# Optimization experiments

Measured on AMD Instinct MI355X. Metric: run time of the kernel, lower is better.

Reference implementation:

```python
import jax, jax.numpy as jnp
import numpy as np

B, S, D, H = 2, 2048, 1024, 16
MASK_VAL = -50000.0

def setup_inputs() -> dict:
    key = jax.random.key(0)
    k1, k2, k3, k4 = jax.random.split(key, 4)
    # weights stored as [in, out] so projection is x @ W (equals torch Linear with W.T)
    s = 1.0 / np.sqrt(D)
    return {
        "x": jax.random.normal(k1, (B, S, D), dtype=jnp.float32),
        "Wq": jax.random.normal(k2, (D, D), dtype=jnp.float32) * s,
        "Wkv": jax.random.normal(k3, (D, 2 * D), dtype=jnp.float32) * s,
        "Wo": jax.random.normal(k4, (D, D), dtype=jnp.float32) * s,
    }

def reference(x, Wq, Wkv, Wo):
    b, sl, d = x.shape
    h = H
    hd = d // h
    scale = hd ** (-0.5)
    q = x @ Wq                      # [b, sl, d]
    kv = x @ Wkv                    # [b, sl, 2d]
    k, v = jnp.split(kv, 2, axis=-1)
    # [b, h, s, hd]
    q = q.reshape(b, sl, h, hd).transpose(0, 2, 1, 3)
    k = k.reshape(b, sl, h, hd).transpose(0, 2, 1, 3)
    v = v.reshape(b, sl, h, hd).transpose(0, 2, 1, 3)
    dots = jnp.einsum('bhid,bhjd->bhij', q * scale, k)  # [b,h,s,s]
    # causal: strictly-upper-triangular entries set to MASK_VAL
    causal = jnp.tril(jnp.ones((sl, sl), dtype=bool))
    dots = jnp.where(causal, dots, MASK_VAL)
    attn = jax.nn.softmax(dots, axis=-1)
    out = jnp.einsum('bhij,bhjd->bihd', attn, v).reshape(b, sl, d)
    return out @ Wo
```

## Files before the change

kernel.cpp:

```cpp
#include <hip/hip_runtime.h>

typedef __bf16 bf16_t;
typedef unsigned short u16;
typedef __attribute__((ext_vector_type(8))) __bf16 bf16x8;
typedef __attribute__((ext_vector_type(4))) float f32x4;
typedef __attribute__((ext_vector_type(4))) u16 u16x4;
typedef __attribute__((ext_vector_type(8))) u16 u16x8;

#define SS 2048
#define PSTR 72

__device__ __forceinline__ u16 f2b(float f) {
    return __builtin_bit_cast(u16, (__bf16)f);
}

__device__ __forceinline__ void async_copy16(const u16* g, u16* l) {
    __builtin_amdgcn_global_load_lds(
        (__attribute__((address_space(1))) void*)(u16*)g,
        (__attribute__((address_space(3))) void*)l, 16, 0, 0);
}

__device__ __forceinline__ bf16x8 ldfrag(const u16* p) {
    return __builtin_bit_cast(bf16x8, *(const u16x8*)p);
}

__global__ __launch_bounds__(256)
void cast_x_kernel(const float* __restrict__ x, u16* __restrict__ xb) {
    size_t i = ((size_t)blockIdx.x * 256 + threadIdx.x) * 8;
    float4 a = *(const float4*)(x + i);
    float4 b = *(const float4*)(x + i + 4);
    u16x8 o;
    o[0] = f2b(a.x); o[1] = f2b(a.y); o[2] = f2b(a.z); o[3] = f2b(a.w);
    o[4] = f2b(b.x); o[5] = f2b(b.y); o[6] = f2b(b.z); o[7] = f2b(b.w);
    *(u16x8*)(xb + i) = o;
}

__global__ __launch_bounds__(256)
void transpose_all(const float* __restrict__ Wq, const float* __restrict__ Wkv,
                   const float* __restrict__ Wo, u16* __restrict__ WcatT,
                   u16* __restrict__ WoT) {
    const int z = blockIdx.z;
    if (z != 1 && blockIdx.y >= 16) return;
    const float* src; u16* dst; int N; float scale;
    if (z == 0)      { src = Wq;  dst = WcatT;               N = 1024; scale = 0.125f * 1.44269504089f; }
    else if (z == 1) { src = Wkv; dst = WcatT + 1024 * 1024; N = 2048; scale = 1.0f; }
    else             { src = Wo;  dst = WoT;                 N = 1024; scale = 1.0f; }
    __shared__ __attribute__((aligned(16))) u16 tile[64][72];
    const int k0 = blockIdx.x * 64, n0 = blockIdx.y * 64;
    const int tid = threadIdx.x;
#pragma unroll
    for (int p = 0; p < 4; ++p) {
        int c = p * 256 + tid;
        int r = c >> 4, c4 = c & 15;
        float4 v = *(const float4*)(src + (size_t)(k0 + r) * N + n0 + c4 * 4);
        u16x4 o;
        o[0] = f2b(v.x * scale); o[1] = f2b(v.y * scale);
        o[2] = f2b(v.z * scale); o[3] = f2b(v.w * scale);
        *(u16x4*)&tile[r][c4 * 4] = o;
    }
    __syncthreads();
#pragma unroll
    for (int p = 0; p < 4; ++p) {
        int c = p * 256 + tid;
        int n = c >> 4, k4 = c & 15;
        u16x4 o;
#pragma unroll
        for (int i = 0; i < 4; ++i) o[i] = tile[k4 * 4 + i][n];
        *(u16x4*)(dst + (size_t)(n0 + n) * 1024 + k0 + k4 * 4) = o;
    }
}

__global__ __launch_bounds__(256)
void transpose_v(const u16* __restrict__ QKV, u16* __restrict__ VTg) {
    __shared__ __attribute__((aligned(16))) u16 tile[64][72];
    const int s0 = blockIdx.x * 64;
    const int bh = blockIdx.y;
    const int b = bh >> 4, h = bh & 15;
    const int tid = threadIdx.x;
    const u16* src = QKV + ((size_t)b * SS + s0) * 3072 + 2048 + h * 64;
#pragma unroll
    for (int p = 0; p < 4; ++p) {
        int c = p * 256 + tid;
        int s = c >> 4, h4 = c & 15;
        *(u16x4*)&tile[s][h4 * 4] = *(const u16x4*)(src + (size_t)s * 3072 + h4 * 4);
    }
    __syncthreads();
    u16* dst = VTg + (size_t)bh * 64 * 2048 + s0;
#pragma unroll
    for (int p = 0; p < 4; ++p) {
        int c = p * 256 + tid;
        int hd = c >> 4, s4 = c & 15;
        u16x4 o;
#pragma unroll
        for (int i = 0; i < 4; ++i) o[i] = tile[s4 * 4 + i][hd];
        *(u16x4*)(dst + (size_t)hd * 2048 + s4 * 4) = o;
    }
}

template <typename OutT>
__global__ __launch_bounds__(256, 2)
void gemm_bt(const u16* __restrict__ A, const u16* __restrict__ BT,
             OutT* __restrict__ C, int M, int N, int K) {
    __shared__ __attribute__((aligned(16))) u16 As[128 * 32];
    __shared__ __attribute__((aligned(16))) u16 Bs[128 * 32];
    const int tid = threadIdx.x;
    const int wave = tid >> 6, lane = tid & 63;
    const int l15 = lane & 15, quad = lane >> 4;
    const int m0 = blockIdx.y * 128, n0 = blockIdx.x * 128;
    const int wm = (wave >> 1) * 64, wn = (wave & 1) * 64;
    const f32x4 zero = {0.f, 0.f, 0.f, 0.f};
    f32x4 acc[4][4];
#pragma unroll
    for (int i = 0; i < 4; ++i)
#pragma unroll
        for (int j = 0; j < 4; ++j) acc[i][j] = zero;
    const int r0 = tid >> 2, kc = (tid & 3) * 8;
    for (int k0 = 0; k0 < K; k0 += 32) {
        async_copy16(A + (size_t)(m0 + r0) * K + k0 + kc, As + tid * 8);
        async_copy16(BT + (size_t)(n0 + r0) * K + k0 + kc, Bs + tid * 8);
        async_copy16(A + (size_t)(m0 + 64 + r0) * K + k0 + kc, As + (256 + tid) * 8);
        async_copy16(BT + (size_t)(n0 + 64 + r0) * K + k0 + kc, Bs + (256 + tid) * 8);
        __syncthreads();
        bf16x8 af[4], bf[4];
#pragma unroll
        for (int t = 0; t < 4; ++t) {
            af[t] = ldfrag(As + (wm + t * 16 + l15) * 32 + quad * 8);
            bf[t] = ldfrag(Bs + (wn + t * 16 + l15) * 32 + quad * 8);
        }
#pragma unroll
        for (int mt = 0; mt < 4; ++mt)
#pragma unroll
            for (int nt = 0; nt < 4; ++nt)
                acc[mt][nt] = __builtin_amdgcn_mfma_f32_16x16x32_bf16(
                    af[mt], bf[nt], acc[mt][nt], 0, 0, 0);
        __syncthreads();
    }
#pragma unroll
    for (int mt = 0; mt < 4; ++mt)
#pragma unroll
        for (int nt = 0; nt < 4; ++nt) {
            const int n = n0 + wn + nt * 16 + l15;
#pragma unroll
            for (int r = 0; r < 4; ++r) {
                const int m = m0 + wm + mt * 16 + quad * 4 + r;
                float v = acc[mt][nt][r];
                if constexpr (sizeof(OutT) == 2) C[(size_t)m * N + n] = (OutT)f2b(v);
                else                             C[(size_t)m * N + n] = v;
            }
        }
}

__device__ __forceinline__ void attn_score_softmax(
    const bf16x8 (&qf)[2], const bf16x8 (&kf)[4][2],
    float (&l_i)[4], u16* __restrict__ P, int wq, int kv0, int l15, int quad) {
    const f32x4 cinit = {-10.f, -10.f, -10.f, -10.f};
    f32x4 S[4];
#pragma unroll
    for (int nt = 0; nt < 4; ++nt) {
        f32x4 a = __builtin_amdgcn_mfma_f32_16x16x32_bf16(qf[0], kf[nt][0], cinit, 0, 0, 0);
        S[nt] = __builtin_amdgcn_mfma_f32_16x16x32_bf16(qf[1], kf[nt][1], a, 0, 0, 0);
    }
    if (kv0 + 63 > wq) {
#pragma unroll
        for (int nt = 0; nt < 4; ++nt)
#pragma unroll
            for (int r = 0; r < 4; ++r) {
                int qa = wq + quad * 4 + r;
                int ka = kv0 + nt * 16 + l15;
                if (ka > qa) S[nt][r] = -1e30f;
            }
    }
#pragma unroll
    for (int nt = 0; nt < 4; ++nt)
#pragma unroll
        for (int r = 0; r < 4; ++r) {
            float pv = exp2f(S[nt][r]);
            l_i[r] += pv;
            P[(quad * 4 + r) * PSTR + nt * 16 + l15] = f2b(pv);
        }
}

__device__ __forceinline__ void attn_pv(
    const u16* __restrict__ P, const bf16x8 (&vf)[4][2],
    f32x4 (&O)[4], int l15, int quad) {
    bf16x8 pf0 = ldfrag(P + l15 * PSTR + quad * 8);
    bf16x8 pf1 = ldfrag(P + l15 * PSTR + 32 + quad * 8);
#pragma unroll
    for (int nt = 0; nt < 4; ++nt) {
        O[nt] = __builtin_amdgcn_mfma_f32_16x16x32_bf16(pf0, vf[nt][0], O[nt], 0, 0, 0);
        O[nt] = __builtin_amdgcn_mfma_f32_16x16x32_bf16(pf1, vf[nt][1], O[nt], 0, 0, 0);
    }
}

__global__ __launch_bounds__(256, 2)
void attn_kernel(const u16* __restrict__ QKV, const u16* __restrict__ VTg,
                 u16* __restrict__ AO) {
    __shared__ __attribute__((aligned(16))) u16 Kt[2][2 * 64 * 32];
    __shared__ __attribute__((aligned(16))) u16 Vt[2][2 * 64 * 32];
    __shared__ __attribute__((aligned(16))) u16 Pq[128 * PSTR];
    const int tid = threadIdx.x;
    const int wave = tid >> 6, lane = tid & 63;
    const int l15 = lane & 15, quad = lane >> 4;
    const int bh = blockIdx.y, b = bh >> 4, h = bh & 15;
    const int xe = b ? 15 - (int)blockIdx.x : (int)blockIdx.x;
    const int qbA = 31 - xe, qbB = xe;
    const int qA0 = qbA * 64, qB0 = qbB * 64;
    const size_t bS = (size_t)b * SS;
    const u16* vbase = VTg + (size_t)bh * 64 * 2048;
    const int rr = (tid >> 2) & 63, kc8 = (tid & 3) * 8;

    {
        const u16* qsrcA = QKV + (bS + qA0 + rr) * 3072 + h * 64 + kc8;
        async_copy16(qsrcA,      Pq + tid * 8);
        async_copy16(qsrcA + 32, Pq + (256 + tid) * 8);
        const u16* qsrcB = QKV + (bS + qB0 + rr) * 3072 + h * 64 + kc8;
        async_copy16(qsrcB,      Pq + (512 + tid) * 8);
        async_copy16(qsrcB + 32, Pq + (768 + tid) * 8);
        const u16* ksrc = QKV + (bS + rr) * 3072 + 1024 + h * 64 + kc8;
        async_copy16(ksrc,      Kt[0] + tid * 8);
        async_copy16(ksrc + 32, Kt[0] + (256 + tid) * 8);
        const u16* vsrc = vbase + (size_t)rr * 2048 + kc8;
        async_copy16(vsrc,      Vt[0] + tid * 8);
        async_copy16(vsrc + 32, Vt[0] + (256 + tid) * 8);
    }
    __syncthreads();
    bf16x8 qfA[2], qfB[2];
#pragma unroll
    for (int ks = 0; ks < 2; ++ks) {
        qfA[ks] = ldfrag(Pq + ks * 2048 + (wave * 16 + l15) * 32 + quad * 8);
        qfB[ks] = ldfrag(Pq + 4096 + ks * 2048 + (wave * 16 + l15) * 32 + quad * 8);
    }
    __syncthreads();

    const int wqA = qA0 + wave * 16, wqB = qB0 + wave * 16;
    u16* PA = Pq + (wave * 16) * PSTR;
    u16* PB = Pq + (64 + wave * 16) * PSTR;
    float lA[4], lB[4];
    f32x4 OA[4], OB[4];
    const f32x4 zero = {0.f, 0.f, 0.f, 0.f};
#pragma unroll
    for (int r = 0; r < 4; ++r) { lA[r] = lB[r] = 0.f; }
#pragma unroll
    for (int nt = 0; nt < 4; ++nt) { OA[nt] = zero; OB[nt] = zero; }

    for (int j = 0; j <= qbA; ++j) {
        if (j < qbA) {
            const int kv1 = (j + 1) * 64;
            const int nb = (j + 1) & 1;
            const u16* ksrc = QKV + (bS + kv1 + rr) * 3072 + 1024 + h * 64 + kc8;
            async_copy16(ksrc,      Kt[nb] + tid * 8);
            async_copy16(ksrc + 32, Kt[nb] + (256 + tid) * 8);
            const u16* vsrc = vbase + (size_t)rr * 2048 + kv1 + kc8;
            async_copy16(vsrc,      Vt[nb] + tid * 8);
            async_copy16(vsrc + 32, Vt[nb] + (256 + tid) * 8);
        }
        const int kv0 = j * 64;
        const bool bAct = (j <= qbB);
        const u16* KB = Kt[j & 1];
        const u16* VB = Vt[j & 1];
        bf16x8 kf[4][2];
#pragma unroll
        for (int nt = 0; nt < 4; ++nt)
#pragma unroll
            for (int ks = 0; ks < 2; ++ks)
                kf[nt][ks] = ldfrag(KB + ks * 2048 + (nt * 16 + l15) * 32 + quad * 8);
        attn_score_softmax(qfA, kf, lA, PA, wqA, kv0, l15, quad);
        if (bAct)
            attn_score_softmax(qfB, kf, lB, PB, wqB, kv0, l15, quad);
        bf16x8 vf[4][2];
#pragma unroll
        for (int nt = 0; nt < 4; ++nt)
#pragma unroll
            for (int ks = 0; ks < 2; ++ks)
                vf[nt][ks] = ldfrag(VB + ks * 2048 + (nt * 16 + l15) * 32 + quad * 8);
        attn_pv(PA, vf, OA, l15, quad);
        if (bAct)
            attn_pv(PB, vf, OB, l15, quad);
        __syncthreads();
    }
#pragma unroll
    for (int r = 0; r < 4; ++r) {
        float sA = lA[r];
        sA += __shfl_xor(sA, 1); sA += __shfl_xor(sA, 2);
        sA += __shfl_xor(sA, 4); sA += __shfl_xor(sA, 8);
        float sB = lB[r];
        sB += __shfl_xor(sB, 1); sB += __shfl_xor(sB, 2);
        sB += __shfl_xor(sB, 4); sB += __shfl_xor(sB, 8);
        float invA = 1.0f / sA;
        float invB = 1.0f / sB;
        size_t rowA = bS + (size_t)wqA + quad * 4 + r;
        size_t rowB = bS + (size_t)wqB + quad * 4 + r;
#pragma unroll
        for (int nt = 0; nt < 4; ++nt) {
            AO[rowA * 1024 + h * 64 + nt * 16 + l15] = f2b(OA[nt][r] * invA);
            AO[rowB * 1024 + h * 64 + nt * 16 + l15] = f2b(OB[nt][r] * invB);
        }
    }
}

extern "C" void kernel_launch(void* const* d_in, const int* in_sizes, int n_in,
                              void* d_out, int out_size, void* d_ws, size_t ws_size,
                              hipStream_t stream) {
    (void)in_sizes; (void)n_in; (void)out_size; (void)ws_size;
    const float* x   = (const float*)d_in[0];
    const float* Wq  = (const float*)d_in[1];
    const float* Wkv = (const float*)d_in[2];
    const float* Wo  = (const float*)d_in[3];
    float* out = (float*)d_out;
    char* ws = (char*)d_ws;
    u16* xb    = (u16*)(ws);
    u16* WcatT = (u16*)(ws + (size_t)(8 << 20));
    u16* WoT   = (u16*)(ws + (size_t)(14 << 20));
    u16* QKV   = (u16*)(ws + (size_t)(16 << 20));
    u16* VTb   = (u16*)(ws + (size_t)(40 << 20));
    u16* AO    = xb;

    cast_x_kernel<<<2048, 256, 0, stream>>>(x, xb);
    transpose_all<<<dim3(16, 32, 3), 256, 0, stream>>>(Wq, Wkv, Wo, WcatT, WoT);
    gemm_bt<u16><<<dim3(24, 32), 256, 0, stream>>>(xb, WcatT, QKV, 4096, 3072, 1024);
    transpose_v<<<dim3(32, 32), 256, 0, stream>>>(QKV, VTb);
    attn_kernel<<<dim3(16, 32), 256, 0, stream>>>(QKV, VTb, AO);
    gemm_bt<float><<<dim3(8, 32), 256, 0, stream>>>(AO, WoT, out, 4096, 1024, 1024);
}
```

Baseline: 195.4 us.

## Split attention KV range across two blocks and add combine kernel

Each attention block pair is split into two halves over the key/value range, doubling the grid and raising the occupancy hint to 4 blocks per CU. Each half writes unnormalized bf16 partial outputs and row sums, and a new combine kernel adds them and normalizes. K/V staging drops from double-buffered prefetch to a single buffer that is loaded and synchronized each iteration, trading latency hiding for lower LDS use. The extra kernel and partial-output traffic add memory cost, and rounding the partials to bf16 adds rounding error.

Measured after the change: 205.5 us. +5.2%, slower.

```diff
diff --git a/kernel.cpp b/kernel.cpp
--- a/kernel.cpp
+++ b/kernel.cpp
@@ -12,6 +12,11 @@
 
 __device__ __forceinline__ u16 f2b(float f) {
     return __builtin_bit_cast(u16, (__bf16)f);
+}
+
+__device__ __forceinline__ float b2f(u16 v) {
+    unsigned u = (unsigned)v << 16;
+    return __builtin_bit_cast(float, u);
 }
 
 __device__ __forceinline__ void async_copy16(const u16* g, u16* l) {
@@ -192,19 +197,23 @@
     }
 }
 
-__global__ __launch_bounds__(256, 2)
+__global__ __launch_bounds__(256, 4)
 void attn_kernel(const u16* __restrict__ QKV, const u16* __restrict__ VTg,
-                 u16* __restrict__ AO) {
-    __shared__ __attribute__((aligned(16))) u16 Kt[2][2 * 64 * 32];
-    __shared__ __attribute__((aligned(16))) u16 Vt[2][2 * 64 * 32];
+                 u16* __restrict__ Opart, float* __restrict__ lpart) {
+    __shared__ __attribute__((aligned(16))) u16 Kt[2 * 64 * 32];
+    __shared__ __attribute__((aligned(16))) u16 Vt[2 * 64 * 32];
     __shared__ __attribute__((aligned(16))) u16 Pq[128 * PSTR];
     const int tid = threadIdx.x;
     const int wave = tid >> 6, lane = tid & 63;
     const int l15 = lane & 15, quad = lane >> 4;
     const int bh = blockIdx.y, b = bh >> 4, h = bh & 15;
-    const int xe = b ? 15 - (int)blockIdx.x : (int)blockIdx.x;
+    const int pair = (int)blockIdx.x >> 1, half = (int)blockIdx.x & 1;
+    const int xe = b ? 15 - pair : pair;
     const int qbA = 31 - xe, qbB = xe;
     const int qA0 = qbA * 64, qB0 = qbB * 64;
+    const int m = (xe >= 8) ? 8 : (15 - xe);
+    const int j0 = half ? m : 0;
+    const int j1 = half ? (qbA + 1) : m;
     const size_t bS = (size_t)b * SS;
     const u16* vbase = VTg + (size_t)bh * 64 * 2048;
     const int rr = (tid >> 2) & 63, kc8 = (tid & 3) * 8;
@@ -216,12 +225,6 @@
         const u16* qsrcB = QKV + (bS + qB0 + rr) * 3072 + h * 64 + kc8;
         async_copy16(qsrcB,      Pq + (512 + tid) * 8);
         async_copy16(qsrcB + 32, Pq + (768 + tid) * 8);
-        const u16* ksrc = QKV + (bS + rr) * 3072 + 1024 + h * 64 + kc8;
-        async_copy16(ksrc,      Kt[0] + tid * 8);
-        async_copy16(ksrc + 32, Kt[0] + (256 + tid) * 8);
-        const u16* vsrc = vbase + (size_t)rr * 2048 + kc8;
-        async_copy16(vsrc,      Vt[0] + tid * 8);
-        async_copy16(vsrc + 32, Vt[0] + (256 + tid) * 8);
     }
     __syncthreads();
     bf16x8 qfA[2], qfB[2];
@@ -243,27 +246,24 @@
 #pragma unroll
     for (int nt = 0; nt < 4; ++nt) { OA[nt] = zero; OB[nt] = zero; }
 
-    for (int j = 0; j <= qbA; ++j) {
-        if (j < qbA) {
-            const int kv1 = (j + 1) * 64;
-            const int nb = (j + 1) & 1;
-            const u16* ksrc = QKV + (bS + kv1 + rr) * 3072 + 1024 + h * 64 + kc8;
-            async_copy16(ksrc,      Kt[nb] + tid * 8);
-            async_copy16(ksrc + 32, Kt[nb] + (256 + tid) * 8);
-            const u16* vsrc = vbase + (size_t)rr * 2048 + kv1 + kc8;
-            async_copy16(vsrc,      Vt[nb] + tid * 8);
-            async_copy16(vsrc + 32, Vt[nb] + (256 + tid) * 8);
-        }
+    for (int j = j0; j < j1; ++j) {
         const int kv0 = j * 64;
+        {
+            const u16* ksrc = QKV + (bS + kv0 + rr) * 3072 + 1024 + h * 64 + kc8;
+            async_copy16(ksrc,      Kt + tid * 8);
+            async_copy16(ksrc + 32, Kt + (256 + tid) * 8);
+            const u16* vsrc = vbase + (size_t)rr * 2048 + kv0 + kc8;
+            async_copy16(vsrc,      Vt + tid * 8);
+            async_copy16(vsrc + 32, Vt + (256 + tid) * 8);
+        }
+        __syncthreads();
         const bool bAct = (j <= qbB);
-        const u16* KB = Kt[j & 1];
-        const u16* VB = Vt[j & 1];
         bf16x8 kf[4][2];
 #pragma unroll
         for (int nt = 0; nt < 4; ++nt)
 #pragma unroll
             for (int ks = 0; ks < 2; ++ks)
-                kf[nt][ks] = ldfrag(KB + ks * 2048 + (nt * 16 + l15) * 32 + quad * 8);
+                kf[nt][ks] = ldfrag(Kt + ks * 2048 + (nt * 16 + l15) * 32 + quad * 8);
         attn_score_softmax(qfA, kf, lA, PA, wqA, kv0, l15, quad);
         if (bAct)
             attn_score_softmax(qfB, kf, lB, PB, wqB, kv0, l15, quad);
@@ -272,12 +272,14 @@
         for (int nt = 0; nt < 4; ++nt)
 #pragma unroll
             for (int ks = 0; ks < 2; ++ks)
-                vf[nt][ks] = ldfrag(VB + ks * 2048 + (nt * 16 + l15) * 32 + quad * 8);
+                vf[nt][ks] = ldfrag(Vt + ks * 2048 + (nt * 16 + l15) * 32 + quad * 8);
         attn_pv(PA, vf, OA, l15, quad);
         if (bAct)
             attn_pv(PB, vf, OB, l15, quad);
         __syncthreads();
     }
+    u16* OpH = Opart + (size_t)half * 4096 * 1024;
+    float* lpH = lpart + (size_t)half * 4096 * 16;
 #pragma unroll
     for (int r = 0; r < 4; ++r) {
         float sA = lA[r];
@@ -286,16 +288,34 @@
         float sB = lB[r];
         sB += __shfl_xor(sB, 1); sB += __shfl_xor(sB, 2);
         sB += __shfl_xor(sB, 4); sB += __shfl_xor(sB, 8);
-        float invA = 1.0f / sA;
-        float invB = 1.0f / sB;
         size_t rowA = bS + (size_t)wqA + quad * 4 + r;
         size_t rowB = bS + (size_t)wqB + quad * 4 + r;
+        if (l15 == 0) {
+            lpH[rowA * 16 + h] = sA;
+            lpH[rowB * 16 + h] = sB;
+        }
 #pragma unroll
         for (int nt = 0; nt < 4; ++nt) {
-            AO[rowA * 1024 + h * 64 + nt * 16 + l15] = f2b(OA[nt][r] * invA);
-            AO[rowB * 1024 + h * 64 + nt * 16 + l15] = f2b(OB[nt][r] * invB);
-        }
-    }
+            OpH[rowA * 1024 + h * 64 + nt * 16 + l15] = f2b(OA[nt][r]);
+            OpH[rowB * 1024 + h * 64 + nt * 16 + l15] = f2b(OB[nt][r]);
+        }
+    }
+}
+
+__global__ __launch_bounds__(256)
+void combine_kernel(const u16* __restrict__ Opart, const float* __restrict__ lpart,
+                    u16* __restrict__ AO) {
+    const size_t idx = ((size_t)blockIdx.x * 256 + threadIdx.x) * 8;
+    const int row = (int)(idx >> 10);
+    const int head = (int)((idx & 1023) >> 6);
+    float l = lpart[row * 16 + head] + lpart[(size_t)4096 * 16 + row * 16 + head];
+    float inv = 1.0f / l;
+    u16x8 a = *(const u16x8*)(Opart + idx);
+    u16x8 c = *(const u16x8*)(Opart + (size_t)4096 * 1024 + idx);
+    u16x8 o;
+#pragma unroll
+    for (int i = 0; i < 8; ++i) o[i] = f2b((b2f(a[i]) + b2f(c[i])) * inv);
+    *(u16x8*)(AO + idx) = o;
 }
 
 extern "C" void kernel_launch(void* const* d_in, const int* in_sizes, int n_in,
@@ -313,12 +333,15 @@
     u16* WoT   = (u16*)(ws + (size_t)(14 << 20));
     u16* QKV   = (u16*)(ws + (size_t)(16 << 20));
     u16* VTb   = (u16*)(ws + (size_t)(40 << 20));
+    u16* Opart = (u16*)(ws + (size_t)(48 << 20));
+    float* lpart = (float*)(ws + (size_t)(64 << 20));
     u16* AO    = xb;
 
     cast_x_kernel<<<2048, 256, 0, stream>>>(x, xb);
     transpose_all<<<dim3(16, 32, 3), 256, 0, stream>>>(Wq, Wkv, Wo, WcatT, WoT);
     gemm_bt<u16><<<dim3(24, 32), 256, 0, stream>>>(xb, WcatT, QKV, 4096, 3072, 1024);
     transpose_v<<<dim3(32, 32), 256, 0, stream>>>(QKV, VTb);
-    attn_kernel<<<dim3(16, 32), 256, 0, stream>>>(QKV, VTb, AO);
+    attn_kernel<<<dim3(32, 32), 256, 0, stream>>>(QKV, VTb, Opart, lpart);
+    combine_kernel<<<2048, 256, 0, stream>>>(Opart, lpart, AO);
     gemm_bt<float><<<dim3(8, 32), 256, 0, stream>>>(AO, WoT, out, 4096, 1024, 1024);
 }
```
